# Kernel tuning notes

Hardware: AMD Instinct MI355X
Metric: run time of the kernel (lower is better)

Reference implementation:

```python
import jax, jax.numpy as jnp
import numpy as np


def _gcs_conv(x, a, w1, w2, b):
    # GCSConv: relu(A @ x W1 + x W2 + b);  x:[B,N,F], a:[B,N,N]
    return jax.nn.relu(jnp.einsum('bij,bjh->bih', a, x @ w1) + x @ w2 + b)


def _topk_pool(x, a, p, ratio=0.5):
    # score y = x . p/||p||, keep top ceil(ratio*N) nodes per graph,
    # gate kept node features with sigmoid(y), slice adjacency rows+cols.
    y = x @ (p / jnp.linalg.norm(p))            # [B, N]
    k = int(np.ceil(ratio * y.shape[1]))
    yk, idx = jax.lax.top_k(y, k)               # [B, k]
    xk = jnp.take_along_axis(x, idx[:, :, None], axis=1)
    xk = xk * jax.nn.sigmoid(yk)[:, :, None]    # gated node features [B,k,H]
    ak = jnp.take_along_axis(a, idx[:, :, None], axis=1)
    ak = jnp.take_along_axis(ak, idx[:, None, :], axis=2)  # [B,k,k]
    return xk, ak


def setup_inputs() -> dict:
    B, N, F0, H, C = 256, 512, 128, 32, 16
    key = jax.random.key(0)
    ks = jax.random.split(key, 12)
    s = lambda fan: 1.0 / np.sqrt(fan)
    return {
        'x': jax.random.normal(ks[0], (B, N, F0), jnp.float32),
        'a': jax.random.uniform(ks[1], (B, N, N), jnp.float32),
        'w1_1': jax.random.normal(ks[2], (F0, H), jnp.float32) * s(F0),
        'w2_1': jax.random.normal(ks[3], (F0, H), jnp.float32) * s(F0),
        'b1': jnp.zeros((H,), jnp.float32),
        'w1_2': jax.random.normal(ks[4], (H, H), jnp.float32) * s(H),
        'w2_2': jax.random.normal(ks[5], (H, H), jnp.float32) * s(H),
        'b2': jnp.zeros((H,), jnp.float32),
        'w1_3': jax.random.normal(ks[6], (H, H), jnp.float32) * s(H),
        'w2_3': jax.random.normal(ks[7], (H, H), jnp.float32) * s(H),
        'b3': jnp.zeros((H,), jnp.float32),
        'p_pool': jax.random.normal(ks[8], (H,), jnp.float32),
        'wd': jax.random.normal(ks[9], (H, C), jnp.float32) * s(H),
        'bd': jnp.zeros((C,), jnp.float32),
    }


def reference(x, a, w1_1, w2_1, b1, w1_2, w2_2, b2, w1_3, w2_3, b3, p_pool, wd, bd):
    x = _gcs_conv(x, a, w1_1, w2_1, b1)
    # NOTE: original code reuses pool1 twice -> shared p_pool for both stages
    x1, a1 = _topk_pool(x, a, p_pool)
    x1 = _gcs_conv(x1, a1, w1_2, w2_2, b2)
    x2, a2 = _topk_pool(x1, a1, p_pool)
    x2 = _gcs_conv(x2, a2, w1_3, w2_3, b3)
    pooled = jnp.mean(x2, axis=1)               # GlobalAvgPool over nodes [B,H]
    return jax.nn.softmax(pooled @ wd + bd, axis=-1)
```

## Files before the change

kernel.cpp:

```cpp
#include <hip/hip_runtime.h>
#include <cmath>

#define B 256
#define N0 512
#define F0 128
#define H 32
#define NC 16

typedef short v8s __attribute__((ext_vector_type(8)));
typedef float v4f __attribute__((ext_vector_type(4)));
typedef unsigned short v8u __attribute__((ext_vector_type(8)));

__device__ inline ushort bf16_rne(float f) {
  unsigned u = __float_as_uint(f);
  unsigned r = (u + 0x7FFF + ((u >> 16) & 1)) >> 16;
  return (ushort)r;
}
__device__ inline float bf16_f(ushort s) { return __uint_as_float((unsigned)s << 16); }

template<int F, int RPT>
__global__ __launch_bounds__(256) void k_xw1(
    const float* __restrict__ x, const float* __restrict__ w1,
    const float* __restrict__ w2, const float* __restrict__ bias,
    ushort* __restrict__ hTh, ushort* __restrict__ hTl, float* __restrict__ g) {
  __shared__ float w1t[H][F + 4];
  __shared__ float w2t[H][F + 4];
  __shared__ float bs[H];
  __shared__ __align__(16) ushort thi[H][72];
  __shared__ __align__(16) ushort tlo[H][72];
  const int tid = threadIdx.x;
  for (int i = tid; i < F * H; i += 256) {
    int f = i >> 5, hc = i & 31;
    w1t[hc][f] = w1[i];
    w2t[hc][f] = w2[i];
  }
  if (tid < H) bs[tid] = bias[tid];
  __syncthreads();
  const int hq = tid & 7;
  const int rq = tid >> 3;
  const size_t row0 = (size_t)blockIdx.x * (32 * RPT) + (size_t)rq * RPT;
  const float* xb = x + row0 * F;
  float acc1[RPT][4];
  float acc2[RPT][4];
  #pragma unroll
  for (int r = 0; r < RPT; ++r)
    for (int c = 0; c < 4; ++c) { acc1[r][c] = 0.f; acc2[r][c] = 0.f; }
  for (int f0 = 0; f0 < F; f0 += 4) {
    float4 w1v[4], w2v[4];
    #pragma unroll
    for (int hh = 0; hh < 4; ++hh) {
      w1v[hh] = *(const float4*)&w1t[hq * 4 + hh][f0];
      w2v[hh] = *(const float4*)&w2t[hq * 4 + hh][f0];
    }
    #pragma unroll
    for (int r = 0; r < RPT; ++r) {
      float4 xv = *(const float4*)(xb + (size_t)r * F + f0);
      #pragma unroll
      for (int hh = 0; hh < 4; ++hh) {
        acc1[r][hh] += xv.x * w1v[hh].x + xv.y * w1v[hh].y + xv.z * w1v[hh].z + xv.w * w1v[hh].w;
        acc2[r][hh] += xv.x * w2v[hh].x + xv.y * w2v[hh].y + xv.z * w2v[hh].z + xv.w * w2v[hh].w;
      }
    }
  }
  #pragma unroll
  for (int r = 0; r < RPT; ++r) {
    size_t o = (row0 + r) * H + hq * 4;
    *(float4*)(g + o) = make_float4(acc2[r][0] + bs[hq * 4 + 0], acc2[r][1] + bs[hq * 4 + 1],
                                    acc2[r][2] + bs[hq * 4 + 2], acc2[r][3] + bs[hq * 4 + 3]);
    #pragma unroll
    for (int c = 0; c < 4; ++c) {
      float v = acc1[r][c];
      ushort hi = bf16_rne(v);
      thi[hq * 4 + c][rq * RPT + r] = hi;
      tlo[hq * 4 + c][rq * RPT + r] = bf16_rne(v - bf16_f(hi));
    }
  }
  __syncthreads();
  const int b = blockIdx.x >> 3;
  const int j0 = (blockIdx.x & 7) * 64;
  const int hrow = tid >> 3, seg = tid & 7;
  size_t o = ((size_t)b * H + hrow) * N0 + j0 + seg * 8;
  *(uint4*)&hTh[o] = *(const uint4*)&thi[hrow][seg * 8];
  *(uint4*)&hTl[o] = *(const uint4*)&tlo[hrow][seg * 8];
}

template<int NPREV, int K, int RPT>
__global__ __launch_bounds__(256) void k_xwg(
    const float* __restrict__ xsrc, const int* __restrict__ lidx,
    const float* __restrict__ gate,
    const float* __restrict__ w1, const float* __restrict__ w2,
    const float* __restrict__ bias,
    float* __restrict__ h, float* __restrict__ g) {
  constexpr int F = H;
  __shared__ float w1t[H][F + 4];
  __shared__ float w2t[H][F + 4];
  __shared__ float bs[H];
  const int tid = threadIdx.x;
  for (int i = tid; i < F * H; i += 256) {
    int f = i >> 5, hc = i & 31;
    w1t[hc][f] = w1[i];
    w2t[hc][f] = w2[i];
  }
  if (tid < H) bs[tid] = bias[tid];
  __syncthreads();
  const int hq = tid & 7;
  const int rq = tid >> 3;
  const int row0 = blockIdx.x * (32 * RPT) + rq * RPT;
  const int b = row0 / K;
  const float* xg0 = xsrc + (size_t)b * NPREV * H;
  int li[RPT];
  float gt[RPT];
  #pragma unroll
  for (int r = 0; r < RPT; ++r) { li[r] = lidx[row0 + r]; gt[r] = gate[row0 + r]; }
  float acc1[RPT][4];
  float acc2[RPT][4];
  #pragma unroll
  for (int r = 0; r < RPT; ++r)
    for (int c = 0; c < 4; ++c) { acc1[r][c] = 0.f; acc2[r][c] = 0.f; }
  for (int f0 = 0; f0 < F; f0 += 4) {
    float4 w1v[4], w2v[4];
    #pragma unroll
    for (int hh = 0; hh < 4; ++hh) {
      w1v[hh] = *(const float4*)&w1t[hq * 4 + hh][f0];
      w2v[hh] = *(const float4*)&w2t[hq * 4 + hh][f0];
    }
    #pragma unroll
    for (int r = 0; r < RPT; ++r) {
      float4 xv = *(const float4*)(xg0 + (size_t)li[r] * H + f0);
      #pragma unroll
      for (int hh = 0; hh < 4; ++hh) {
        acc1[r][hh] += xv.x * w1v[hh].x + xv.y * w1v[hh].y + xv.z * w1v[hh].z + xv.w * w1v[hh].w;
        acc2[r][hh] += xv.x * w2v[hh].x + xv.y * w2v[hh].y + xv.z * w2v[hh].z + xv.w * w2v[hh].w;
      }
    }
  }
  #pragma unroll
  for (int r = 0; r < RPT; ++r) {
    size_t o = ((size_t)row0 + r) * H + hq * 4;
    *(float4*)(h + o) = make_float4(acc1[r][0] * gt[r], acc1[r][1] * gt[r],
                                    acc1[r][2] * gt[r], acc1[r][3] * gt[r]);
    *(float4*)(g + o) = make_float4(acc2[r][0] * gt[r] + bs[hq * 4 + 0],
                                    acc2[r][1] * gt[r] + bs[hq * 4 + 1],
                                    acc2[r][2] * gt[r] + bs[hq * 4 + 2],
                                    acc2[r][3] * gt[r] + bs[hq * 4 + 3]);
  }
}

template<int K>
__global__ __launch_bounds__(512) void k_trans_inv(
    const float* __restrict__ hd, const int* __restrict__ idx,
    ushort* __restrict__ hTh, ushort* __restrict__ hTl) {
  __shared__ float hs[K][33];
  __shared__ int inv[N0];
  const int tid = threadIdx.x;
  const int b = blockIdx.x;
  for (int j = tid; j < N0; j += 512) inv[j] = -1;
  __syncthreads();
  for (int k = tid; k < K; k += 512) inv[idx[(size_t)b * K + k]] = k;
  for (int t = tid; t < K * 8; t += 512) {
    int r = t >> 3, c4 = t & 7;
    float4 v = *(const float4*)(hd + (((size_t)b * K) + r) * H + c4 * 4);
    hs[r][c4 * 4 + 0] = v.x;
    hs[r][c4 * 4 + 1] = v.y;
    hs[r][c4 * 4 + 2] = v.z;
    hs[r][c4 * 4 + 3] = v.w;
  }
  __syncthreads();
  for (int t = tid; t < H * 64; t += 512) {
    int hr = t >> 6, seg = t & 63;
    v8u hv, lv;
    #pragma unroll
    for (int i = 0; i < 8; ++i) {
      int k = inv[seg * 8 + i];
      float v = (k >= 0) ? hs[k][hr] : 0.f;
      ushort hi = bf16_rne(v);
      hv[i] = hi;
      lv[i] = bf16_rne(v - bf16_f(hi));
    }
    size_t o = ((size_t)b * H + hr) * N0 + seg * 8;
    *(v8u*)&hTh[o] = hv;
    *(v8u*)&hTl[o] = lv;
  }
}

template<int NROW>
__global__ __launch_bounds__(256) void k_ammx(
    const float* __restrict__ a0, const int* __restrict__ rid,
    const ushort* __restrict__ hTh, const ushort* __restrict__ hTl,
    const float* __restrict__ g, const float* __restrict__ p,
    float* __restrict__ out, float* __restrict__ yout) {
  constexpr int RB = 64;
  constexpr int KC = 32;
  constexpr int ASP = KC + 8;
  __shared__ ushort ah[RB][ASP];
  __shared__ ushort al[RB][ASP];
  __shared__ ushort bh[H][ASP];
  __shared__ ushort bl[H][ASP];
  __shared__ int rowid[RB];
  __shared__ float psu[H];
  __shared__ float pns_s;
  const int tid = threadIdx.x;
  const int b = blockIdx.x;
  const int row0 = blockIdx.y * RB;
  if (tid < RB) rowid[tid] = rid ? rid[(size_t)b * NROW + row0 + tid] : row0 + tid;
  if (yout && tid == 0) {
    float s = 0.f;
    for (int i = 0; i < H; ++i) s += p[i] * p[i];
    pns_s = 1.f / sqrtf(s);
  }
  __syncthreads();
  if (yout && tid < H) psu[tid] = p[tid] * pns_s;
  const int wave = tid >> 6, lane = tid & 63;
  const int m = lane & 15, quad = lane >> 4;
  const int sr = tid >> 2, skq = tid & 3;
  const int shh = tid >> 3, sseg = tid & 7;
  const float* abase = a0 + (size_t)b * N0 * N0;
  const ushort* bhsrc = hTh + ((size_t)b * H + shh) * N0 + sseg * 4;
  const ushort* blsrc = hTl + ((size_t)b * H + shh) * N0 + sseg * 4;
  v4f acc0 = {0.f, 0.f, 0.f, 0.f};
  v4f acc1 = {0.f, 0.f, 0.f, 0.f};
  for (int k0 = 0; k0 < N0; k0 += KC) {
    if (k0) __syncthreads();
    {
      const float* ap = abase + (size_t)rowid[sr] * N0 + k0 + skq * 4;
      float4 v0 = *(const float4*)ap;
      float4 v1 = *(const float4*)(ap + 16);
      ushort4 h0, l0, h1, l1;
      h0.x = bf16_rne(v0.x); l0.x = bf16_rne(v0.x - bf16_f(h0.x));
      h0.y = bf16_rne(v0.y); l0.y = bf16_rne(v0.y - bf16_f(h0.y));
      h0.z = bf16_rne(v0.z); l0.z = bf16_rne(v0.z - bf16_f(h0.z));
      h0.w = bf16_rne(v0.w); l0.w = bf16_rne(v0.w - bf16_f(h0.w));
      h1.x = bf16_rne(v1.x); l1.x = bf16_rne(v1.x - bf16_f(h1.x));
      h1.y = bf16_rne(v1.y); l1.y = bf16_rne(v1.y - bf16_f(h1.y));
      h1.z = bf16_rne(v1.z); l1.z = bf16_rne(v1.z - bf16_f(h1.z));
      h1.w = bf16_rne(v1.w); l1.w = bf16_rne(v1.w - bf16_f(h1.w));
      *(ushort4*)&ah[sr][skq * 4] = h0;      *(ushort4*)&al[sr][skq * 4] = l0;
      *(ushort4*)&ah[sr][skq * 4 + 16] = h1; *(ushort4*)&al[sr][skq * 4 + 16] = l1;
    }
    {
      *(ushort4*)&bh[shh][sseg * 4] = *(const ushort4*)(bhsrc + k0);
      *(ushort4*)&bl[shh][sseg * 4] = *(const ushort4*)(blsrc + k0);
    }
    __syncthreads();
    const int arow = wave * 16 + m;
    v8s Ah = *(const v8s*)&ah[arow][quad * 8];
    v8s Al = *(const v8s*)&al[arow][quad * 8];
    v8s Bh0 = *(const v8s*)&bh[m][quad * 8];
    v8s Bh1 = *(const v8s*)&bh[16 + m][quad * 8];
    v8s Bl0 = *(const v8s*)&bl[m][quad * 8];
    v8s Bl1 = *(const v8s*)&bl[16 + m][quad * 8];
    acc0 = __builtin_amdgcn_mfma_f32_16x16x32_bf16(Ah, Bh0, acc0, 0, 0, 0);
    acc1 = __builtin_amdgcn_mfma_f32_16x16x32_bf16(Ah, Bh1, acc1, 0, 0, 0);
    acc0 = __builtin_amdgcn_mfma_f32_16x16x32_bf16(Al, Bh0, acc0, 0, 0, 0);
    acc1 = __builtin_amdgcn_mfma_f32_16x16x32_bf16(Al, Bh1, acc1, 0, 0, 0);
    acc0 = __builtin_amdgcn_mfma_f32_16x16x32_bf16(Ah, Bl0, acc0, 0, 0, 0);
    acc1 = __builtin_amdgcn_mfma_f32_16x16x32_bf16(Ah, Bl1, acc1, 0, 0, 0);
  }
  float part[4];
  #pragma unroll
  for (int reg = 0; reg < 4; ++reg) {
    int row = row0 + wave * 16 + quad * 4 + reg;
    size_t o0 = ((size_t)b * NROW + row) * H + m;
    size_t o1 = o0 + 16;
    float v0 = fmaxf(acc0[reg] + g[o0], 0.f);
    float v1 = fmaxf(acc1[reg] + g[o1], 0.f);
    out[o0] = v0;
    out[o1] = v1;
    if (yout) part[reg] = v0 * psu[m] + v1 * psu[m + 16];
  }
  if (yout) {
    #pragma unroll
    for (int reg = 0; reg < 4; ++reg)
      #pragma unroll
      for (int off = 1; off < 16; off <<= 1)
        part[reg] += __shfl_xor(part[reg], off, 16);
    if (m < 4)
      yout[(size_t)b * NROW + row0 + wave * 16 + quad * 4 + m] = part[m];
  }
}

template<int NN, int K>
__global__ __launch_bounds__(256) void k_topk(
    const float* __restrict__ y, const int* __restrict__ prev_idx,
    int* __restrict__ lidx, float* __restrict__ gate, int* __restrict__ out_idx) {
  __shared__ float ys[NN];
  __shared__ int is[NN];
  const int tid = threadIdx.x;
  const int b = blockIdx.x;
  for (int i = tid; i < NN; i += 256) {
    ys[i] = y[(size_t)b * NN + i];
    is[i] = i;
  }
  for (int k = 2; k <= NN; k <<= 1) {
    for (int j = k >> 1; j > 0; j >>= 1) {
      __syncthreads();
      for (int i = tid; i < NN; i += 256) {
        int ixj = i ^ j;
        if (ixj > i) {
          float v0 = ys[i], v1 = ys[ixj];
          int i0 = is[i], i1 = is[ixj];
          bool pre = (v1 > v0) || (v1 == v0 && i1 < i0);
          bool doswap = ((i & k) == 0) ? pre : !pre;
          if (doswap) { ys[i] = v1; ys[ixj] = v0; is[i] = i1; is[ixj] = i0; }
        }
      }
    }
  }
  for (int k = 2; k <= K; k <<= 1) {
    for (int j = k >> 1; j > 0; j >>= 1) {
      __syncthreads();
      for (int i = tid; i < K; i += 256) {
        int ixj = i ^ j;
        if (ixj > i && ixj < K) {
          float v0 = ys[i], v1 = ys[ixj];
          int i0 = is[i], i1 = is[ixj];
          bool pre = (i1 < i0);
          bool doswap = ((i & k) == 0) ? pre : !pre;
          if (doswap) { ys[i] = v1; ys[ixj] = v0; is[i] = i1; is[ixj] = i0; }
        }
      }
    }
  }
  __syncthreads();
  for (int t = tid; t < K; t += 256) {
    lidx[(size_t)b * K + t] = is[t];
    gate[(size_t)b * K + t] = 1.f / (1.f + expf(-ys[t]));
    out_idx[(size_t)b * K + t] = prev_idx ? prev_idx[(size_t)b * NN + is[t]] : is[t];
  }
}

__global__ __launch_bounds__(128) void k_head(
    const float* __restrict__ xl3, const float* __restrict__ wd,
    const float* __restrict__ bd, float* __restrict__ out) {
  __shared__ float part[4][H];
  __shared__ float pooled[H];
  __shared__ float wds[H * NC];
  __shared__ float logits[NC];
  const int tid = threadIdx.x;
  const int b = blockIdx.x;
  for (int i = tid; i < H * NC; i += 128) wds[i] = wd[i];
  const int f = tid & 31, nq = tid >> 5;
  float s = 0.f;
  for (int n = nq * 32; n < nq * 32 + 32; ++n)
    s += xl3[((size_t)b * 128 + n) * H + f];
  part[nq][f] = s;
  __syncthreads();
  if (tid < H)
    pooled[tid] = (part[0][tid] + part[1][tid] + part[2][tid] + part[3][tid]) * (1.f / 128.f);
  __syncthreads();
  if (tid < NC) {
    float acc = bd[tid];
    for (int i = 0; i < H; ++i) acc += pooled[i] * wds[i * NC + tid];
    logits[tid] = acc;
  }
  __syncthreads();
  if (tid == 0) {
    float mx = logits[0];
    for (int i = 1; i < NC; ++i) mx = fmaxf(mx, logits[i]);
    float e[NC], se = 0.f;
    for (int i = 0; i < NC; ++i) { e[i] = expf(logits[i] - mx); se += e[i]; }
    float inv = 1.f / se;
    for (int i = 0; i < NC; ++i) out[(size_t)b * NC + i] = e[i] * inv;
  }
}

extern "C" void kernel_launch(void* const* d_in, const int* in_sizes, int n_in,
                              void* d_out, int out_size, void* d_ws, size_t ws_size,
                              hipStream_t stream) {
  (void)in_sizes; (void)n_in; (void)out_size; (void)ws_size;
  const float* x    = (const float*)d_in[0];
  const float* a    = (const float*)d_in[1];
  const float* w1_1 = (const float*)d_in[2];
  const float* w2_1 = (const float*)d_in[3];
  const float* b1   = (const float*)d_in[4];
  const float* w1_2 = (const float*)d_in[5];
  const float* w2_2 = (const float*)d_in[6];
  const float* b2   = (const float*)d_in[7];
  const float* w1_3 = (const float*)d_in[8];
  const float* w2_3 = (const float*)d_in[9];
  const float* b3   = (const float*)d_in[10];
  const float* pp   = (const float*)d_in[11];
  const float* wd   = (const float*)d_in[12];
  const float* bd   = (const float*)d_in[13];
  float* out = (float*)d_out;

  char* w = (char*)d_ws;
  auto take = [&](size_t bytes) { char* r = w; w += (bytes + 255) & ~(size_t)255; return r; };
  ushort* hTh = (ushort*)take((size_t)B * H * N0 * 2);
  ushort* hTl = (ushort*)take((size_t)B * H * N0 * 2);
  float*  g1  = (float*) take((size_t)B * N0 * H * 4);
  float*  xl1 = (float*) take((size_t)B * N0 * H * 4);
  float*  y1  = (float*) take((size_t)B * N0 * 4);
  int*    id1 = (int*)   take((size_t)B * 256 * 4);
  int*    li1 = (int*)   take((size_t)B * 256 * 4);
  float*  gt1 = (float*) take((size_t)B * 256 * 4);
  float*  h2  = (float*) take((size_t)B * 256 * H * 4);
  float*  g2  = (float*) take((size_t)B * 256 * H * 4);
  float*  xl2 = (float*) take((size_t)B * 256 * H * 4);
  float*  y2  = (float*) take((size_t)B * 256 * 4);
  int*    id2 = (int*)   take((size_t)B * 128 * 4);
  int*    li2 = (int*)   take((size_t)B * 128 * 4);
  float*  gt2 = (float*) take((size_t)B * 128 * 4);
  float*  h3  = (float*) take((size_t)B * 128 * H * 4);
  float*  g3  = (float*) take((size_t)B * 128 * H * 4);
  float*  xl3 = (float*) take((size_t)B * 128 * H * 4);

  k_xw1<F0, 2><<<dim3(B * N0 / 64), dim3(256), 0, stream>>>(x, w1_1, w2_1, b1, hTh, hTl, g1);
  k_ammx<512><<<dim3(B, 8), dim3(256), 0, stream>>>(a, nullptr, hTh, hTl, g1, pp, xl1, y1);
  k_topk<512, 256><<<dim3(B), dim3(256), 0, stream>>>(y1, nullptr, li1, gt1, id1);
  k_xwg<512, 256, 4><<<dim3(B * 256 / 128), dim3(256), 0, stream>>>(xl1, li1, gt1, w1_2, w2_2, b2, h2, g2);
  k_trans_inv<256><<<dim3(B), dim3(512), 0, stream>>>(h2, id1, hTh, hTl);
  k_ammx<256><<<dim3(B, 4), dim3(256), 0, stream>>>(a, id1, hTh, hTl, g2, pp, xl2, y2);
  k_topk<256, 128><<<dim3(B), dim3(256), 0, stream>>>(y2, id1, li2, gt2, id2);
  k_xwg<256, 128, 4><<<dim3(B * 128 / 128), dim3(256), 0, stream>>>(xl2, li2, gt2, w1_3, w2_3, b3, h3, g3);
  k_trans_inv<128><<<dim3(B), dim3(512), 0, stream>>>(h3, id2, hTh, hTl);
  k_ammx<128><<<dim3(B, 2), dim3(256), 0, stream>>>(a, id2, hTh, hTl, g3, nullptr, xl3, nullptr);
  k_head<<<dim3(B), dim3(128), 0, stream>>>(xl3, wd, bd, out);
}
```

Baseline: 585.4 us.

## Fuse xwg with transpose-scatter and register-prefetch A/B chunks in ammx

Merges the gated X·W kernel with the inverse-index transpose/bf16-split kernel so the h intermediate stays in shared memory instead of round-tripping through global memory, and removes two launches. The ammx kernel's K chunk grows from 32 to 64, and it prefetches the next chunk of A and hT into registers before the barrier, so global loads overlap the split and MFMA work. The cost is one block per graph in the fused kernel (fewer, larger blocks with RPT of 8 or 4), plus higher register and LDS use in ammx.

```diff
diff --git a/kernel.cpp b/kernel.cpp
--- a/kernel.cpp
+++ b/kernel.cpp
@@ -84,34 +84,42 @@
   *(uint4*)&hTl[o] = *(const uint4*)&tlo[hrow][seg * 8];
 }
 
-template<int NPREV, int K, int RPT>
-__global__ __launch_bounds__(256) void k_xwg(
+template<int NPREV, int K>
+__global__ __launch_bounds__(256) void k_xwg2(
     const float* __restrict__ xsrc, const int* __restrict__ lidx,
-    const float* __restrict__ gate,
+    const float* __restrict__ gate, const int* __restrict__ gidx,
     const float* __restrict__ w1, const float* __restrict__ w2,
     const float* __restrict__ bias,
-    float* __restrict__ h, float* __restrict__ g) {
+    float* __restrict__ g, ushort* __restrict__ hTh, ushort* __restrict__ hTl) {
   constexpr int F = H;
+  constexpr int RPT = K / 32;
   __shared__ float w1t[H][F + 4];
   __shared__ float w2t[H][F + 4];
   __shared__ float bs[H];
+  __shared__ float hs[K][36];
+  __shared__ int inv[N0];
   const int tid = threadIdx.x;
+  const int b = blockIdx.x;
   for (int i = tid; i < F * H; i += 256) {
     int f = i >> 5, hc = i & 31;
     w1t[hc][f] = w1[i];
     w2t[hc][f] = w2[i];
   }
   if (tid < H) bs[tid] = bias[tid];
-  __syncthreads();
+  for (int j = tid; j < N0; j += 256) inv[j] = -1;
+  __syncthreads();
+  for (int k = tid; k < K; k += 256) inv[gidx[(size_t)b * K + k]] = k;
   const int hq = tid & 7;
   const int rq = tid >> 3;
-  const int row0 = blockIdx.x * (32 * RPT) + rq * RPT;
-  const int b = row0 / K;
+  const int r0 = rq * RPT;
   const float* xg0 = xsrc + (size_t)b * NPREV * H;
   int li[RPT];
   float gt[RPT];
   #pragma unroll
-  for (int r = 0; r < RPT; ++r) { li[r] = lidx[row0 + r]; gt[r] = gate[row0 + r]; }
+  for (int r = 0; r < RPT; ++r) {
+    li[r] = lidx[(size_t)b * K + r0 + r];
+    gt[r] = gate[(size_t)b * K + r0 + r];
+  }
   float acc1[RPT][4];
   float acc2[RPT][4];
   #pragma unroll
@@ -136,43 +144,22 @@
   }
   #pragma unroll
   for (int r = 0; r < RPT; ++r) {
-    size_t o = ((size_t)row0 + r) * H + hq * 4;
-    *(float4*)(h + o) = make_float4(acc1[r][0] * gt[r], acc1[r][1] * gt[r],
-                                    acc1[r][2] * gt[r], acc1[r][3] * gt[r]);
+    size_t o = ((size_t)b * K + r0 + r) * H + hq * 4;
     *(float4*)(g + o) = make_float4(acc2[r][0] * gt[r] + bs[hq * 4 + 0],
                                     acc2[r][1] * gt[r] + bs[hq * 4 + 1],
                                     acc2[r][2] * gt[r] + bs[hq * 4 + 2],
                                     acc2[r][3] * gt[r] + bs[hq * 4 + 3]);
-  }
-}
-
-template<int K>
-__global__ __launch_bounds__(512) void k_trans_inv(
-    const float* __restrict__ hd, const int* __restrict__ idx,
-    ushort* __restrict__ hTh, ushort* __restrict__ hTl) {
-  __shared__ float hs[K][33];
-  __shared__ int inv[N0];
-  const int tid = threadIdx.x;
-  const int b = blockIdx.x;
-  for (int j = tid; j < N0; j += 512) inv[j] = -1;
-  __syncthreads();
-  for (int k = tid; k < K; k += 512) inv[idx[(size_t)b * K + k]] = k;
-  for (int t = tid; t < K * 8; t += 512) {
-    int r = t >> 3, c4 = t & 7;
-    float4 v = *(const float4*)(hd + (((size_t)b * K) + r) * H + c4 * 4);
-    hs[r][c4 * 4 + 0] = v.x;
-    hs[r][c4 * 4 + 1] = v.y;
-    hs[r][c4 * 4 + 2] = v.z;
-    hs[r][c4 * 4 + 3] = v.w;
-  }
-  __syncthreads();
-  for (int t = tid; t < H * 64; t += 512) {
+    *(float4*)&hs[r0 + r][hq * 4] = make_float4(acc1[r][0] * gt[r], acc1[r][1] * gt[r],
+                                                acc1[r][2] * gt[r], acc1[r][3] * gt[r]);
+  }
+  __syncthreads();
+  for (int t = tid; t < H * 64; t += 256) {
     int hr = t >> 6, seg = t & 63;
     v8u hv, lv;
     #pragma unroll
     for (int i = 0; i < 8; ++i) {
-      int k = inv[seg * 8 + i];
-      float v = (k >= 0) ? hs[k][hr] : 0.f;
+      int kk = inv[seg * 8 + i];
+      float v = (kk >= 0) ? hs[kk][hr] : 0.f;
       ushort hi = bf16_rne(v);
       hv[i] = hi;
       lv[i] = bf16_rne(v - bf16_f(hi));
@@ -190,7 +177,8 @@
     const float* __restrict__ g, const float* __restrict__ p,
     float* __restrict__ out, float* __restrict__ yout) {
   constexpr int RB = 64;
-  constexpr int KC = 32;
+  constexpr int KC = 64;
+  constexpr int NCH = N0 / KC;
   constexpr int ASP = KC + 8;
   __shared__ ushort ah[RB][ASP];
   __shared__ ushort al[RB][ASP];
@@ -214,47 +202,58 @@
   const int m = lane & 15, quad = lane >> 4;
   const int sr = tid >> 2, skq = tid & 3;
   const int shh = tid >> 3, sseg = tid & 7;
-  const float* abase = a0 + (size_t)b * N0 * N0;
-  const ushort* bhsrc = hTh + ((size_t)b * H + shh) * N0 + sseg * 4;
-  const ushort* blsrc = hTl + ((size_t)b * H + shh) * N0 + sseg * 4;
+  const float* ap = a0 + (size_t)b * N0 * N0 + (size_t)rowid[sr] * N0 + skq * 4;
+  const ushort* bhsrc = hTh + ((size_t)b * H + shh) * N0 + sseg * 8;
+  const ushort* blsrc = hTl + ((size_t)b * H + shh) * N0 + sseg * 8;
   v4f acc0 = {0.f, 0.f, 0.f, 0.f};
   v4f acc1 = {0.f, 0.f, 0.f, 0.f};
-  for (int k0 = 0; k0 < N0; k0 += KC) {
-    if (k0) __syncthreads();
-    {
-      const float* ap = abase + (size_t)rowid[sr] * N0 + k0 + skq * 4;
-      float4 v0 = *(const float4*)ap;
-      float4 v1 = *(const float4*)(ap + 16);
-      ushort4 h0, l0, h1, l1;
-      h0.x = bf16_rne(v0.x); l0.x = bf16_rne(v0.x - bf16_f(h0.x));
-      h0.y = bf16_rne(v0.y); l0.y = bf16_rne(v0.y - bf16_f(h0.y));
-      h0.z = bf16_rne(v0.z); l0.z = bf16_rne(v0.z - bf16_f(h0.z));
-      h0.w = bf16_rne(v0.w); l0.w = bf16_rne(v0.w - bf16_f(h0.w));
-      h1.x = bf16_rne(v1.x); l1.x = bf16_rne(v1.x - bf16_f(h1.x));
-      h1.y = bf16_rne(v1.y); l1.y = bf16_rne(v1.y - bf16_f(h1.y));
-      h1.z = bf16_rne(v1.z); l1.z = bf16_rne(v1.z - bf16_f(h1.z));
-      h1.w = bf16_rne(v1.w); l1.w = bf16_rne(v1.w - bf16_f(h1.w));
-      *(ushort4*)&ah[sr][skq * 4] = h0;      *(ushort4*)&al[sr][skq * 4] = l0;
-      *(ushort4*)&ah[sr][skq * 4 + 16] = h1; *(ushort4*)&al[sr][skq * 4 + 16] = l1;
-    }
-    {
-      *(ushort4*)&bh[shh][sseg * 4] = *(const ushort4*)(bhsrc + k0);
-      *(ushort4*)&bl[shh][sseg * 4] = *(const ushort4*)(blsrc + k0);
-    }
+  float4 rA[2][4];
+  uint4 rBh[2], rBl[2];
+  #pragma unroll
+  for (int i = 0; i < 4; ++i) rA[0][i] = *(const float4*)(ap + i * 16);
+  rBh[0] = *(const uint4*)bhsrc;
+  rBl[0] = *(const uint4*)blsrc;
+  #pragma unroll
+  for (int c = 0; c < NCH; ++c) {
+    const int cur = c & 1, nxt = cur ^ 1;
+    if (c + 1 < NCH) {
+      #pragma unroll
+      for (int i = 0; i < 4; ++i)
+        rA[nxt][i] = *(const float4*)(ap + (c + 1) * KC + i * 16);
+      rBh[nxt] = *(const uint4*)(bhsrc + (c + 1) * KC);
+      rBl[nxt] = *(const uint4*)(blsrc + (c + 1) * KC);
+    }
+    if (c) __syncthreads();
+    #pragma unroll
+    for (int i = 0; i < 4; ++i) {
+      float4 v = rA[cur][i];
+      ushort4 hh, ll;
+      hh.x = bf16_rne(v.x); ll.x = bf16_rne(v.x - bf16_f(hh.x));
+      hh.y = bf16_rne(v.y); ll.y = bf16_rne(v.y - bf16_f(hh.y));
+      hh.z = bf16_rne(v.z); ll.z = bf16_rne(v.z - bf16_f(hh.z));
+      hh.w = bf16_rne(v.w); ll.w = bf16_rne(v.w - bf16_f(hh.w));
+      *(ushort4*)&ah[sr][i * 16 + skq * 4] = hh;
+      *(ushort4*)&al[sr][i * 16 + skq * 4] = ll;
+    }
+    *(uint4*)&bh[shh][sseg * 8] = rBh[cur];
+    *(uint4*)&bl[shh][sseg * 8] = rBl[cur];
     __syncthreads();
     const int arow = wave * 16 + m;
-    v8s Ah = *(const v8s*)&ah[arow][quad * 8];
-    v8s Al = *(const v8s*)&al[arow][quad * 8];
-    v8s Bh0 = *(const v8s*)&bh[m][quad * 8];
-    v8s Bh1 = *(const v8s*)&bh[16 + m][quad * 8];
-    v8s Bl0 = *(const v8s*)&bl[m][quad * 8];
-    v8s Bl1 = *(const v8s*)&bl[16 + m][quad * 8];
-    acc0 = __builtin_amdgcn_mfma_f32_16x16x32_bf16(Ah, Bh0, acc0, 0, 0, 0);
-    acc1 = __builtin_amdgcn_mfma_f32_16x16x32_bf16(Ah, Bh1, acc1, 0, 0, 0);
-    acc0 = __builtin_amdgcn_mfma_f32_16x16x32_bf16(Al, Bh0, acc0, 0, 0, 0);
-    acc1 = __builtin_amdgcn_mfma_f32_16x16x32_bf16(Al, Bh1, acc1, 0, 0, 0);
-    acc0 = __builtin_amdgcn_mfma_f32_16x16x32_bf16(Ah, Bl0, acc0, 0, 0, 0);
-    acc1 = __builtin_amdgcn_mfma_f32_16x16x32_bf16(Ah, Bl1, acc1, 0, 0, 0);
+    #pragma unroll
+    for (int ks = 0; ks < 2; ++ks) {
+      v8s Ah  = *(const v8s*)&ah[arow][ks * 32 + quad * 8];
+      v8s Al  = *(const v8s*)&al[arow][ks * 32 + quad * 8];
+      v8s Bh0 = *(const v8s*)&bh[m][ks * 32 + quad * 8];
+      v8s Bh1 = *(const v8s*)&bh[16 + m][ks * 32 + quad * 8];
+      v8s Bl0 = *(const v8s*)&bl[m][ks * 32 + quad * 8];
+      v8s Bl1 = *(const v8s*)&bl[16 + m][ks * 32 + quad * 8];
+      acc0 = __builtin_amdgcn_mfma_f32_16x16x32_bf16(Ah, Bh0, acc0, 0, 0, 0);
+      acc1 = __builtin_amdgcn_mfma_f32_16x16x32_bf16(Ah, Bh1, acc1, 0, 0, 0);
+      acc0 = __builtin_amdgcn_mfma_f32_16x16x32_bf16(Al, Bh0, acc0, 0, 0, 0);
+      acc1 = __builtin_amdgcn_mfma_f32_16x16x32_bf16(Al, Bh1, acc1, 0, 0, 0);
+      acc0 = __builtin_amdgcn_mfma_f32_16x16x32_bf16(Ah, Bl0, acc0, 0, 0, 0);
+      acc1 = __builtin_amdgcn_mfma_f32_16x16x32_bf16(Ah, Bl1, acc1, 0, 0, 0);
+    }
   }
   float part[4];
   #pragma unroll
@@ -394,26 +393,22 @@
   int*    id1 = (int*)   take((size_t)B * 256 * 4);
   int*    li1 = (int*)   take((size_t)B * 256 * 4);
   float*  gt1 = (float*) take((size_t)B * 256 * 4);
-  float*  h2  = (float*) take((size_t)B * 256 * H * 4);
   float*  g2  = (float*) take((size_t)B * 256 * H * 4);
   float*  xl2 = (float*) take((size_t)B * 256 * H * 4);
   float*  y2  = (float*) take((size_t)B * 256 * 4);
   int*    id2 = (int*)   take((size_t)B * 128 * 4);
   int*    li2 = (int*)   take((size_t)B * 128 * 4);
   float*  gt2 = (float*) take((size_t)B * 128 * 4);
-  float*  h3  = (float*) take((size_t)B * 128 * H * 4);
   float*  g3  = (float*) take((size_t)B * 128 * H * 4);
   float*  xl3 = (float*) take((size_t)B * 128 * H * 4);
 
   k_xw1<F0, 2><<<dim3(B * N0 / 64), dim3(256), 0, stream>>>(x, w1_1, w2_1, b1, hTh, hTl, g1);
   k_ammx<512><<<dim3(B, 8), dim3(256), 0, stream>>>(a, nullptr, hTh, hTl, g1, pp, xl1, y1);
   k_topk<512, 256><<<dim3(B), dim3(256), 0, stream>>>(y1, nullptr, li1, gt1, id1);
-  k_xwg<512, 256, 4><<<dim3(B * 256 / 128), dim3(256), 0, stream>>>(xl1, li1, gt1, w1_2, w2_2, b2, h2, g2);
-  k_trans_inv<256><<<dim3(B), dim3(512), 0, stream>>>(h2, id1, hTh, hTl);
+  k_xwg2<512, 256><<<dim3(B), dim3(256), 0, stream>>>(xl1, li1, gt1, id1, w1_2, w2_2, b2, g2, hTh, hTl);
   k_ammx<256><<<dim3(B, 4), dim3(256), 0, stream>>>(a, id1, hTh, hTl, g2, pp, xl2, y2);
   k_topk<256, 128><<<dim3(B), dim3(256), 0, stream>>>(y2, id1, li2, gt2, id2);
-  k_xwg<256, 128, 4><<<dim3(B * 128 / 128), dim3(256), 0, stream>>>(xl2, li2, gt2, w1_3, w2_3, b3, h3, g3);
-  k_trans_inv<128><<<dim3(B), dim3(512), 0, stream>>>(h3, id2, hTh, hTl);
+  k_xwg2<256, 128><<<dim3(B), dim3(256), 0, stream>>>(xl2, li2, gt2, id2, w1_3, w2_3, b3, g3, hTh, hTl);
   k_ammx<128><<<dim3(B, 2), dim3(256), 0, stream>>>(a, id2, hTh, hTl, g3, nullptr, xl3, nullptr);
   k_head<<<dim3(B), dim3(128), 0, stream>>>(xl3, wd, bd, out);
 }
```

Measured after the change: 628.8 us. +7.4%, slower.
